# Kernel optimization log

Hardware: AMD Instinct MI355X
Metric: run time of the kernel (lower is better)

Reference implementation:

```python
import jax, jax.numpy as jnp
import numpy as np

K = 10          # n_near
BN_EPS = 1e-5   # BatchNorm eps; running stats at init: mean=0, var=1


def knn_idx(xt, k):
    # xt: [b, n, c] -> [b, n, k] indices of k nearest (incl. self)
    sq = jnp.sum(xt * xt, axis=-1)                               # [b, n]
    d = sq[:, :, None] - 2.0 * jnp.einsum('bnc,bmc->bnm', xt, xt) + sq[:, None, :]
    return jax.lax.top_k(-d, k)[1]                               # [b, n, k]


def graph_feature(x, k):
    # x: [b, c, n] -> [b, 2c, n, k]  (DGCNN edge features)
    xt = x.transpose(0, 2, 1)                                    # [b, n, c]
    idx = knn_idx(xt, k)                                         # [b, n, k]
    nei = jnp.take_along_axis(xt[:, None, :, :], idx[..., None], axis=2)  # [b, n, k, c]
    cen = xt[:, :, None, :]                                      # [b, n, 1, c]
    feat = jnp.concatenate([nei - cen, jnp.broadcast_to(cen, nei.shape)], axis=-1)
    return feat.transpose(0, 3, 1, 2)                            # [b, 2c, n, k]


def conv_bn_act(x, w, b, g, t):
    # 1x1 conv (any spatial rank) + inference BatchNorm (mean=0, var=1) + GELU
    sh = (1, -1) + (1,) * (x.ndim - 2)
    y = jnp.einsum('oi,bi...->bo...', w, x) + b.reshape(sh)
    y = y * (g.reshape(sh) / jnp.sqrt(1.0 + BN_EPS)) + t.reshape(sh)
    return jax.nn.gelu(y)


def setup_inputs() -> dict:
    key = jax.random.key(0)
    ks = jax.random.split(key, 8)
    d = {'x': jax.random.normal(ks[0], (8, 64, 2048), jnp.float32)}
    dims = {'11': (152, 128), '12': (181, 152), '21': (430, 362),
            '22': (512, 430), '31': (595, 693), '32': (512, 595)}
    for i, (tag, (o, inp)) in enumerate(dims.items()):
        d['w' + tag] = jax.random.normal(jax.random.fold_in(key, i + 1), (o, inp), jnp.float32) * 0.02
        d['b' + tag] = jnp.zeros((o,), jnp.float32)
        d['g' + tag] = jnp.ones((o,), jnp.float32)
        d['t' + tag] = jnp.zeros((o,), jnp.float32)
    return d


def reference(x, w11, b11, g11, t11, w12, b12, g12, t12,
              w21, b21, g21, t21, w22, b22, g22, t22,
              w31, b31, g31, t31, w32, b32, g32, t32):
    f = graph_feature(x, K)                       # [b, 128, n, k]
    f = conv_bn_act(f, w11, b11, g11, t11)
    f = conv_bn_act(f, w12, b12, g12, t12)        # [b, 181, n, k]
    x1 = jnp.max(f, axis=-1)                      # [b, 181, n]
    f = graph_feature(x1, K)                      # [b, 362, n, k]
    f = conv_bn_act(f, w21, b21, g21, t21)
    f = conv_bn_act(f, w22, b22, g22, t22)        # [b, 512, n, k]
    x2 = jnp.max(f, axis=-1)                      # [b, 512, n]
    f = jnp.concatenate([x1, x2], axis=1)         # [b, 693, n]
    f = conv_bn_act(f, w31, b31, g31, t31)
    f = conv_bn_act(f, w32, b32, g32, t32)        # [b, 512, n]
    return f
```

## Files before the change

kernel.cpp:

```cpp
#include <hip/hip_runtime.h>


typedef float f4 __attribute__((ext_vector_type(4)));
typedef float f32x4 __attribute__((ext_vector_type(4)));
typedef short bf16x8 __attribute__((ext_vector_type(8)));

#define BNRSQ 0.9999950000374997f

__device__ __forceinline__ float gelu_f(float x){
  float a = 0.7978845608028654f * (x + 0.044715f * x * x * x);
  float e = __expf(2.0f * a);
  float t = 1.0f - 2.0f / (e + 1.0f);
  return 0.5f * x * (1.0f + t);
}

__device__ __forceinline__ short f2b(float x){
  unsigned u = __float_as_uint(x);
  unsigned r = (u + 0x7fffu + ((u >> 16) & 1u)) >> 16;
  return (short)r;
}
__device__ __forceinline__ float b2f(short s){
  return __uint_as_float(((unsigned)(unsigned short)s) << 16);
}

__global__ void makewt_k(const float* __restrict__ W, float* __restrict__ dst,
                         int O, int Cin, int Cpad, int ld, int split){
  int id = blockIdx.x * 256 + threadIdx.x;
  if (id >= Cpad * O) return;
  int c = id / O;
  int o = id - c * O;
  float v = 0.f;
  if (c < Cin){
    float w0 = W[(size_t)o * ld + c];
    v = split ? (W[(size_t)o * ld + Cin + c] - w0) : w0;
  }
  dst[id] = v;
}

__global__ void makew12r_k(const float* __restrict__ w12, float* __restrict__ Wr){
  int id = blockIdx.x * 256 + threadIdx.x;
  if (id >= 38 * 192 * 4) return;
  int i = id & 3;
  int c = (id >> 2) % 192;
  int kq = id / 768;
  int k = kq * 4 + i;
  float v = 0.f;
  if (c < 181 && k < 152) v = w12[(size_t)c * 152 + k];
  Wr[id] = v;
}

__global__ void makewsb_k(const float* __restrict__ W, short* __restrict__ dst){
  int n = blockIdx.x;
  int k = threadIdx.x;
  if (k >= 192) return;
  short v = 0;
  if (k < 181){
    if (n < 430) v = f2b(W[(size_t)n * 362 + k]);
    else if (n >= 448 && n < 878){
      int m = n - 448;
      v = f2b(W[(size_t)m * 362 + 181 + k] - W[(size_t)m * 362 + k]);
    }
  }
  dst[(size_t)n * 192 + k] = v;
}

__global__ void makewb_k(const float* __restrict__ W, short* __restrict__ dst,
                         int N, int K, int Kpad){
  int n = blockIdx.y;
  int k = blockIdx.x * 256 + threadIdx.x;
  if (k >= Kpad) return;
  short v = 0;
  if (n < N && k < K) v = f2b(W[(size_t)n * K + k]);
  dst[(size_t)n * Kpad + k] = v;
}

__global__ __launch_bounds__(256) void transpose_k(const float* __restrict__ x, float* __restrict__ xt){
  __shared__ float tile[64][65];
  int b = blockIdx.y;
  int n0 = blockIdx.x * 64;
  int t = threadIdx.x;
  int a = t & 63, r = t >> 6;
  #pragma unroll
  for (int s = 0; s < 16; s++){
    int c = r + s * 4;
    tile[c][a] = x[((size_t)b * 64 + c) * 2048 + n0 + a];
  }
  __syncthreads();
  #pragma unroll
  for (int s = 0; s < 16; s++){
    int n = r + s * 4;
    xt[((size_t)b * 2048 + n0 + n) * 64 + a] = tile[a][n];
  }
}

__global__ __launch_bounds__(256) void sqnorm_k(const float* __restrict__ X, float* __restrict__ sq,
                                                int C, int ld, int npts){
  int gid = blockIdx.x * blockDim.x + threadIdx.x;
  int wid = gid >> 6, lane = gid & 63;
  if (wid >= npts) return;
  const float* row = X + (size_t)wid * ld;
  float s = 0.f;
  for (int c = lane; c < C; c += 64){ float v = row[c]; s += v * v; }
  #pragma unroll
  for (int off = 32; off; off >>= 1) s += __shfl_xor(s, off);
  if (lane == 0) sq[wid] = s;
}

__global__ __launch_bounds__(256) void dist_k(const float* __restrict__ X, const float* __restrict__ sq,
                                              float* __restrict__ dist, int C, int ldx){
  __shared__ float As[16][132];
  __shared__ float Bs[16][132];
  const int z = blockIdx.z;
  const float* Xb = X + (size_t)z * 2048 * ldx;
  const float* sqb = sq + (z << 11);
  float* db = dist + (size_t)z * 2048 * 2048;
  const int i0 = blockIdx.y * 128, j0 = blockIdx.x * 128;
  const int t = threadIdx.x;
  const int ti = t >> 4, tj = t & 15;
  const int r = t & 127, q8 = (t >> 7) * 8;
  float acc[2][2][4][4];
  #pragma unroll
  for (int a = 0; a < 2; a++)
    #pragma unroll
    for (int b = 0; b < 2; b++)
      #pragma unroll
      for (int u = 0; u < 4; u++)
        #pragma unroll
        for (int v = 0; v < 4; v++) acc[a][b][u][v] = 0.f;
  const float* Ag = Xb + (size_t)(i0 + r) * ldx + q8;
  const float* Bg = Xb + (size_t)(j0 + r) * ldx + q8;
  for (int c0 = 0; c0 < C; c0 += 16){
    f4 av0 = *(const f4*)(Ag + c0);
    f4 av1 = *(const f4*)(Ag + c0 + 4);
    f4 bv0 = *(const f4*)(Bg + c0);
    f4 bv1 = *(const f4*)(Bg + c0 + 4);
    __syncthreads();
    #pragma unroll
    for (int i = 0; i < 4; i++){
      As[q8 + i][r] = av0[i];  As[q8 + 4 + i][r] = av1[i];
      Bs[q8 + i][r] = bv0[i];  Bs[q8 + 4 + i][r] = bv1[i];
    }
    __syncthreads();
    #pragma unroll
    for (int k = 0; k < 16; k++){
      f4 a0 = *(const f4*)&As[k][ti * 4];
      f4 a1 = *(const f4*)&As[k][ti * 4 + 64];
      f4 b0 = *(const f4*)&Bs[k][tj * 4];
      f4 b1 = *(const f4*)&Bs[k][tj * 4 + 64];
      #pragma unroll
      for (int u = 0; u < 4; u++)
        #pragma unroll
        for (int v = 0; v < 4; v++){
          acc[0][0][u][v] += a0[u] * b0[v];
          acc[0][1][u][v] += a0[u] * b1[v];
          acc[1][0][u][v] += a1[u] * b0[v];
          acc[1][1][u][v] += a1[u] * b1[v];
        }
    }
  }
  #pragma unroll
  for (int ia = 0; ia < 2; ia++){
    #pragma unroll
    for (int u = 0; u < 4; u++){
      int i = i0 + ia * 64 + ti * 4 + u;
      float si = sqb[i];
      #pragma unroll
      for (int jb = 0; jb < 2; jb++){
        int j = j0 + jb * 64 + tj * 4;
        f4 o;
        #pragma unroll
        for (int v = 0; v < 4; v++) o[v] = si + sqb[j + v] - 2.0f * acc[ia][jb][u][v];
        *(f4*)&db[(size_t)i * 2048 + j] = o;
      }
    }
  }
}

__global__ __launch_bounds__(256) void topk_k(const float* __restrict__ dist, int* __restrict__ idxout){
  int z = blockIdx.y;
  int lane = threadIdx.x & 63;
  int row = blockIdx.x * 4 + (threadIdx.x >> 6);
  const float* d = dist + (size_t)z * 2048 * 2048 + (size_t)row * 2048;
  float v[32];
  #pragma unroll
  for (int s = 0; s < 32; s++) v[s] = d[s * 64 + lane];
  int* outp = idxout + (size_t)z * 20480 + (size_t)row * 10;
  for (int it = 0; it < 10; ++it){
    float bv = 3.0e38f; int bi = 0x7fffffff;
    #pragma unroll
    for (int s = 0; s < 32; s++){
      if (v[s] < bv){ bv = v[s]; bi = s * 64 + lane; }
    }
    #pragma unroll
    for (int off = 32; off; off >>= 1){
      float ov = __shfl_xor(bv, off);
      int   oi = __shfl_xor(bi, off);
      if (ov < bv || (ov == bv && oi < bi)){ bv = ov; bi = oi; }
    }
    #pragma unroll
    for (int s = 0; s < 32; s++) if (s * 64 + lane == bi) v[s] = 3.0e38f;
    if (lane == 0) outp[it] = bi;
  }
}

__global__ __launch_bounds__(256) void yz_k(const float* __restrict__ Amat, int C,
                                            const float* __restrict__ B1, const float* __restrict__ B2,
                                            int O, float* __restrict__ Y, float* __restrict__ Z){
  __shared__ float As[16][68];
  __shared__ float B1s[16][68];
  __shared__ float B2s[16][68];
  int m0 = blockIdx.y * 64, o0 = blockIdx.x * 64;
  int t = threadIdx.x;
  int cc = t & 15, rr = t >> 4;
  int oo = t & 63, kk = t >> 6;
  float accY[4][4], accZ[4][4];
  #pragma unroll
  for (int u = 0; u < 4; u++)
    #pragma unroll
    for (int v = 0; v < 4; v++){ accY[u][v] = 0.f; accZ[u][v] = 0.f; }
  for (int c0 = 0; c0 < C; c0 += 16){
    #pragma unroll
    for (int u = 0; u < 4; u++){
      int ii = rr + u * 16;
      As[cc][ii] = ((c0 + cc) < C) ? Amat[(size_t)(m0 + ii) * C + c0 + cc] : 0.f;
    }
    #pragma unroll
    for (int u = 0; u < 4; u++){
      int c = kk * 4 + u;
      bool ok = ((c0 + c) < C) && ((o0 + oo) < O);
      B1s[c][oo] = ok ? B1[(size_t)(c0 + c) * O + o0 + oo] : 0.f;
      B2s[c][oo] = ok ? B2[(size_t)(c0 + c) * O + o0 + oo] : 0.f;
    }
    __syncthreads();
    #pragma unroll
    for (int k = 0; k < 16; k++){
      f4 a  = *(const f4*)&As[k][rr * 4];
      f4 b1 = *(const f4*)&B1s[k][cc * 4];
      f4 b2 = *(const f4*)&B2s[k][cc * 4];
      #pragma unroll
      for (int u = 0; u < 4; u++)
        #pragma unroll
        for (int v = 0; v < 4; v++){
          accY[u][v] += a[u] * b1[v];
          accZ[u][v] += a[u] * b2[v];
        }
    }
    __syncthreads();
  }
  #pragma unroll
  for (int u = 0; u < 4; u++){
    int m = m0 + rr * 4 + u;
    #pragma unroll
    for (int v = 0; v < 4; v++){
      int o = o0 + cc * 4 + v;
      if (o < O){
        Y[(size_t)m * O + o] = accY[u][v];
        Z[(size_t)m * O + o] = accZ[u][v];
      }
    }
  }
}

__global__ __launch_bounds__(256) void fused1_k(
    const float* __restrict__ Y1, const float* __restrict__ Z1,
    const int* __restrict__ idx, const float* __restrict__ Wr12,
    const float* __restrict__ bb11, const float* __restrict__ gg11, const float* __restrict__ tt11,
    const float* __restrict__ bb12, const float* __restrict__ gg12, const float* __restrict__ tt12,
    float* __restrict__ x1t, short* __restrict__ x1b, float* __restrict__ sq2){
  __shared__ float h1[40][152];
  __shared__ int sidx[40];
  const int n0 = blockIdx.x * 4;
  const int t = threadIdx.x;
  if (t < 40) sidx[t] = idx[(size_t)n0 * 10 + t];
  __syncthreads();
  const int base = (n0 >> 11) << 11;
  {
    const int tc = t & 63, tr = t >> 6;
    for (int c = tc; c < 152; c += 64){
      float bb = bb11[c], sc = gg11[c] * BNRSQ, tb = tt11[c];
      for (int r = tr; r < 40; r += 4){
        int p = r / 10;
        int j = base + sidx[r];
        float y = Y1[(size_t)j * 152 + c] + Z1[(size_t)(n0 + p) * 152 + c];
        h1[r][c] = gelu_f((y + bb) * sc + tb);
      }
    }
  }
  __syncthreads();
  const int p = t >> 6, kh = (t >> 5) & 1, cg = t & 31;
  const int rbase = p * 10 + kh * 5;
  float acc[5][6];
  #pragma unroll
  for (int k = 0; k < 5; k++)
    #pragma unroll
    for (int j = 0; j < 6; j++) acc[k][j] = 0.f;
  for (int kq = 0; kq < 38; kq++){
    const float* wp = Wr12 + ((size_t)kq * 192 + cg) * 4;
    f4 wv[6];
    #pragma unroll
    for (int j = 0; j < 6; j++) wv[j] = *(const f4*)(wp + j * 128);
    f4 hv[5];
    #pragma unroll
    for (int k = 0; k < 5; k++) hv[k] = *(const f4*)&h1[rbase + k][kq * 4];
    #pragma unroll
    for (int k = 0; k < 5; k++)
      #pragma unroll
      for (int j = 0; j < 6; j++)
        acc[k][j] += hv[k][0] * wv[j][0] + hv[k][1] * wv[j][1]
                   + hv[k][2] * wv[j][2] + hv[k][3] * wv[j][3];
  }
  float ssum = 0.f;
  #pragma unroll
  for (int j = 0; j < 6; j++){
    int c = cg + j * 32;
    float m = 0.f;
    if (c < 181){
      float bb = bb12[c], sc = gg12[c] * BNRSQ, tb = tt12[c];
      m = -3.0e38f;
      #pragma unroll
      for (int k = 0; k < 5; k++){
        float v = gelu_f((acc[k][j] + bb) * sc + tb);
        m = fmaxf(m, v);
      }
    }
    float o = __shfl_xor(m, 32);
    m = fmaxf(m, o);
    if (kh == 0){
      float mv = (c < 181) ? m : 0.f;
      x1t[(size_t)(n0 + p) * 192 + c] = mv;
      x1b[(size_t)(n0 + p) * 192 + c] = f2b(mv);
      ssum += mv * mv;
    }
  }
  #pragma unroll
  for (int off = 16; off; off >>= 1) ssum += __shfl_xor(ssum, off);
  if (kh == 0 && cg == 0) sq2[n0 + p] = ssum;
}

__global__ __launch_bounds__(256) void h2_k(
    const float* __restrict__ YZ, const int* __restrict__ idx,
    const float* __restrict__ bb21, const float* __restrict__ gg21, const float* __restrict__ tt21,
    short* __restrict__ H2){
  __shared__ int sidx[10];
  int bl = blockIdx.x;
  int t = threadIdx.x;
  if (t < 10) sidx[t] = ((bl >> 11) << 11) + idx[(size_t)bl * 10 + t];
  __syncthreads();
  int cA = t;
  int cB = t + 256;
  float zA = YZ[(size_t)bl * 896 + 448 + cA] + bb21[cA];
  float scA = gg21[cA] * BNRSQ, tbA = tt21[cA];
  float zB = 0.f, scB = 0.f, tbB = 0.f;
  bool realB = cB < 430, padB = cB < 448;
  if (realB){
    zB = YZ[(size_t)bl * 896 + 448 + cB] + bb21[cB];
    scB = gg21[cB] * BNRSQ; tbB = tt21[cB];
  }
  #pragma unroll
  for (int k = 0; k < 10; k++){
    int nb = sidx[k];
    size_t rb = ((size_t)bl * 10 + k) * 448;
    float yA = YZ[(size_t)nb * 896 + cA] + zA;
    H2[rb + cA] = f2b(gelu_f(yA * scA + tbA));
    if (padB){
      short v = 0;
      if (realB){
        float yB = YZ[(size_t)nb * 896 + cB] + zB;
        v = f2b(gelu_f(yB * scB + tbB));
      }
      H2[rb + cB] = v;
    }
  }
}

template<int MODE>
__global__ __launch_bounds__(256) void gemm_k(const short* __restrict__ A,
                                              const short* __restrict__ Bt,
                                              int Kp, int Nld, int Nreal,
                                              const float* __restrict__ bv,
                                              const float* __restrict__ gv,
                                              const float* __restrict__ tv,
                                              void* __restrict__ outp){
  __shared__ short As[128][40];
  __shared__ short Bs[128][40];
  const int t = threadIdx.x;
  const int w = t >> 6, l = t & 63;
  const int m0 = blockIdx.y * 128, n0 = blockIdx.x * 128;
  f32x4 acc[2][8];
  #pragma unroll
  for (int i = 0; i < 2; i++)
    #pragma unroll
    for (int j = 0; j < 8; j++) acc[i][j] = (f32x4)0.f;
  const int ar = t >> 2, akc = t & 3;
  const short* Ag0 = A + (size_t)(m0 + ar) * Kp + akc * 8;
  const short* Ag1 = A + (size_t)(m0 + 64 + ar) * Kp + akc * 8;
  const short* Bg0 = Bt + (size_t)(n0 + ar) * Kp + akc * 8;
  const short* Bg1 = Bt + (size_t)(n0 + 64 + ar) * Kp + akc * 8;
  const int mrow = w * 32 + (l & 15);
  const int kg = (l >> 4) * 8;
  const int cl = l & 15;
  for (int k0 = 0; k0 < Kp; k0 += 32){
    int4 va0 = *(const int4*)(Ag0 + k0);
    int4 va1 = *(const int4*)(Ag1 + k0);
    int4 vb0 = *(const int4*)(Bg0 + k0);
    int4 vb1 = *(const int4*)(Bg1 + k0);
    __syncthreads();
    *(int4*)&As[ar][akc * 8]      = va0;
    *(int4*)&As[ar + 64][akc * 8] = va1;
    *(int4*)&Bs[ar][akc * 8]      = vb0;
    *(int4*)&Bs[ar + 64][akc * 8] = vb1;
    __syncthreads();
    bf16x8 a0 = *(const bf16x8*)&As[mrow][kg];
    bf16x8 a1 = *(const bf16x8*)&As[mrow + 16][kg];
    #pragma unroll
    for (int ni = 0; ni < 8; ni++){
      bf16x8 b = *(const bf16x8*)&Bs[cl + ni * 16][kg];
      acc[0][ni] = __builtin_amdgcn_mfma_f32_16x16x32_bf16(a0, b, acc[0][ni], 0, 0, 0);
      acc[1][ni] = __builtin_amdgcn_mfma_f32_16x16x32_bf16(a1, b, acc[1][ni], 0, 0, 0);
    }
  }
  const int rbase = (l >> 4) * 4;
  #pragma unroll
  for (int ni = 0; ni < 8; ni++){
    int n = n0 + ni * 16 + cl;
    float bb = 0.f, sc = 0.f, tb = 0.f;
    if (MODE != 2 && n < Nreal){ bb = bv[n]; sc = gv[n] * BNRSQ; tb = tv[n]; }
    #pragma unroll
    for (int mi = 0; mi < 2; mi++){
      #pragma unroll
      for (int r = 0; r < 4; r++){
        int m = m0 + w * 32 + mi * 16 + rbase + r;
        float a = acc[mi][ni][r];
        float v = (MODE == 2) ? a : gelu_f((a + bb) * sc + tb);
        if (MODE == 0) ((short*)outp)[(size_t)m * Nld + n] = f2b(v);
        else           ((float*)outp)[(size_t)m * Nld + n] = v;
      }
    }
  }
}

__global__ __launch_bounds__(256) void kmax_k(const short* __restrict__ Pb, short* __restrict__ x2b){
  int p = blockIdx.x;
  int t = threadIdx.x;
  #pragma unroll
  for (int j = 0; j < 2; j++){
    int o = t + j * 256;
    float m = -3.0e38f;
    #pragma unroll
    for (int k = 0; k < 10; k++) m = fmaxf(m, b2f(Pb[((size_t)p * 10 + k) * 512 + o]));
    x2b[(size_t)p * 512 + o] = f2b(m);
  }
}

__global__ __launch_bounds__(256) void fcat_k(const float* __restrict__ x1t, const short* __restrict__ x2b,
                                              short* __restrict__ F){
  size_t g = blockIdx.x;
  int t = threadIdx.x;
  for (int c = t; c < 704; c += 256){
    short v = 0;
    if (c < 181) v = f2b(x1t[g * 192 + c]);
    else if (c < 693) v = x2b[g * 512 + (c - 181)];
    F[g * 704 + c] = v;
  }
}

__global__ __launch_bounds__(256) void trout_k(const float* __restrict__ H6, float* __restrict__ out){
  __shared__ float tile[64][65];
  int b = blockIdx.z;
  int nc = blockIdx.x * 64, oc = blockIdx.y * 64;
  int t = threadIdx.x;
  int a = t & 63, r = t >> 6;
  #pragma unroll
  for (int s = 0; s < 16; s++){
    int nl = r + s * 4;
    tile[nl][a] = H6[((size_t)b * 2048 + nc + nl) * 512 + oc + a];
  }
  __syncthreads();
  #pragma unroll
  for (int s = 0; s < 16; s++){
    int ol = r + s * 4;
    out[((size_t)(b * 512 + oc + ol)) * 2048 + nc + a] = tile[a][ol];
  }
}

extern "C" void kernel_launch(void* const* d_in, const int* in_sizes, int n_in,
                              void* d_out, int out_size, void* d_ws, size_t ws_size,
                              hipStream_t stream) {
  const float* x   = (const float*)d_in[0];
  const float* w11 = (const float*)d_in[1];
  const float* b11 = (const float*)d_in[2];
  const float* g11 = (const float*)d_in[3];
  const float* t11 = (const float*)d_in[4];
  const float* w12 = (const float*)d_in[5];
  const float* b12 = (const float*)d_in[6];
  const float* g12 = (const float*)d_in[7];
  const float* t12 = (const float*)d_in[8];
  const float* w21 = (const float*)d_in[9];
  const float* b21 = (const float*)d_in[10];
  const float* g21 = (const float*)d_in[11];
  const float* t21 = (const float*)d_in[12];
  const float* w22 = (const float*)d_in[13];
  const float* b22 = (const float*)d_in[14];
  const float* g22 = (const float*)d_in[15];
  const float* t22 = (const float*)d_in[16];
  const float* w31 = (const float*)d_in[17];
  const float* b31 = (const float*)d_in[18];
  const float* g31 = (const float*)d_in[19];
  const float* t31 = (const float*)d_in[20];
  const float* w32 = (const float*)d_in[21];
  const float* b32 = (const float*)d_in[22];
  const float* g32 = (const float*)d_in[23];
  const float* t32 = (const float*)d_in[24];
  float* out = (float*)d_out;
  char* ws = (char*)d_ws;

  size_t off = 0;
  auto alloc = [&](size_t nbytes) -> char* {
    char* p = ws + off;
    off += ((nbytes + 255) & ~(size_t)255);
    return p;
  };
  float* x1t  = (float*)alloc((size_t)16384 * 192 * 4);
  short* x1b  = (short*)alloc((size_t)16384 * 192 * 2);
  short* x2b  = (short*)alloc((size_t)16384 * 512 * 2);
  float* sq1  = (float*)alloc(65536);
  float* sq2  = (float*)alloc(65536);
  int*   idx1 = (int*)  alloc(655360);
  int*   idx2 = (int*)  alloc(655360);
  float* WaT11 = (float*)alloc(64 * 152 * 4);
  float* WdT11 = (float*)alloc(64 * 152 * 4);
  float* Wr12  = (float*)alloc(38 * 192 * 4 * 4);
  short* W21sb = (short*)alloc((size_t)896 * 192 * 2);
  short* W22b  = (short*)alloc((size_t)512 * 448 * 2);
  short* W31b  = (short*)alloc((size_t)640 * 704 * 2);
  short* W32b  = (short*)alloc((size_t)512 * 640 * 2);
  char* arena = ws + off;
  const size_t ARENA = 93323264;
  if (off + ARENA > ws_size) return;
  float* distP = (float*)(arena);
  float* Y1    = (float*)(arena + 67108864);
  float* Z1    = (float*)(arena + 77070336);
  float* xt    = (float*)(arena + 87031808);
  short* Pb    = (short*)(arena);
  short* H2b   = (short*)(arena + 41943040);
  float* YZ2g  = (float*)(arena + 78643200);
  short* F     = (short*)(arena);
  short* H5    = (short*)(arena + 23068672);
  float* H6    = (float*)(arena + 44040192);

  auto mk = [&](const float* W, float* dst, int O, int Cin, int Cpad, int ld, int split){
    int n = Cpad * O;
    makewt_k<<<dim3((n + 255) / 256), dim3(256), 0, stream>>>(W, dst, O, Cin, Cpad, ld, split);
  };
  mk(w11, WaT11, 152, 64, 64, 128, 0);
  mk(w11, WdT11, 152, 64, 64, 128, 1);
  makew12r_k<<<dim3(114), dim3(256), 0, stream>>>(w12, Wr12);
  makewsb_k<<<dim3(896), dim3(256), 0, stream>>>(w21, W21sb);
  makewb_k<<<dim3(2, 512), dim3(256), 0, stream>>>(w22, W22b, 512, 430, 448);
  makewb_k<<<dim3(3, 640), dim3(256), 0, stream>>>(w31, W31b, 595, 693, 704);
  makewb_k<<<dim3(3, 512), dim3(256), 0, stream>>>(w32, W32b, 512, 595, 640);

  transpose_k<<<dim3(32, 8), dim3(256), 0, stream>>>(x, xt);
  sqnorm_k<<<dim3(4096), dim3(256), 0, stream>>>(xt, sq1, 64, 64, 16384);

  for (int pb = 0; pb < 2; pb++){
    dist_k<<<dim3(16, 16, 4), dim3(256), 0, stream>>>(xt + (size_t)pb * 4 * 2048 * 64,
                                                      sq1 + pb * 8192, distP, 64, 64);
    topk_k<<<dim3(512, 4), dim3(256), 0, stream>>>(distP, idx1 + (size_t)pb * 4 * 20480);
  }
  yz_k<<<dim3(3, 256), dim3(256), 0, stream>>>(xt, 64, WaT11, WdT11, 152, Y1, Z1);
  fused1_k<<<dim3(4096), dim3(256), 0, stream>>>(Y1, Z1, idx1, Wr12,
                                                 b11, g11, t11, b12, g12, t12,
                                                 x1t, x1b, sq2);

  for (int pb = 0; pb < 2; pb++){
    dist_k<<<dim3(16, 16, 4), dim3(256), 0, stream>>>(x1t + (size_t)pb * 4 * 2048 * 192,
                                                      sq2 + pb * 8192, distP, 192, 192);
    topk_k<<<dim3(512, 4), dim3(256), 0, stream>>>(distP, idx2 + (size_t)pb * 4 * 20480);
  }
  for (int g = 0; g < 4; g++){
    gemm_k<2><<<dim3(7, 32), dim3(256), 0, stream>>>(x1b + (size_t)g * 4096 * 192, W21sb,
                                                     192, 896, 896,
                                                     nullptr, nullptr, nullptr, (void*)YZ2g);
    h2_k<<<dim3(4096), dim3(256), 0, stream>>>(YZ2g, idx2 + (size_t)g * 40960,
                                               b21, g21, t21, H2b);
    gemm_k<0><<<dim3(4, 320), dim3(256), 0, stream>>>(H2b, W22b, 448, 512, 512,
                                                      b22, g22, t22, (void*)Pb);
    kmax_k<<<dim3(4096), dim3(256), 0, stream>>>(Pb, x2b + (size_t)g * 4096 * 512);
  }

  fcat_k<<<dim3(16384), dim3(256), 0, stream>>>(x1t, x2b, F);
  gemm_k<0><<<dim3(5, 128), dim3(256), 0, stream>>>(F, W31b, 704, 640, 595,
                                                    b31, g31, t31, (void*)H5);
  gemm_k<1><<<dim3(4, 128), dim3(256), 0, stream>>>(H5, W32b, 640, 512, 512,
                                                    b32, g32, t32, (void*)H6);
  trout_k<<<dim3(32, 8, 8), dim3(256), 0, stream>>>(H6, out);
}
```

Before: 1.098 ms.

## Merge weight-prep kernels into one launch, tune fused1 occupancy and use FMA chain

Seven weight-preparation launches are folded into a single prep kernel that dispatches on block index ranges, which removes per-launch overhead. fused1_k gets a launch bound asking for 4 blocks per SIMD-level occupancy, which may constrain its register allocation. Its inner dot product is rewritten as an explicit chain of fmaf calls. The FMA chain changes the order of the float summation slightly.

```diff
diff --git a/kernel.cpp b/kernel.cpp
--- a/kernel.cpp
+++ b/kernel.cpp
@@ -23,55 +23,68 @@
   return __uint_as_float(((unsigned)(unsigned short)s) << 16);
 }
 
-__global__ void makewt_k(const float* __restrict__ W, float* __restrict__ dst,
-                         int O, int Cin, int Cpad, int ld, int split){
-  int id = blockIdx.x * 256 + threadIdx.x;
-  if (id >= Cpad * O) return;
-  int c = id / O;
-  int o = id - c * O;
-  float v = 0.f;
-  if (c < Cin){
-    float w0 = W[(size_t)o * ld + c];
-    v = split ? (W[(size_t)o * ld + Cin + c] - w0) : w0;
-  }
-  dst[id] = v;
-}
-
-__global__ void makew12r_k(const float* __restrict__ w12, float* __restrict__ Wr){
-  int id = blockIdx.x * 256 + threadIdx.x;
-  if (id >= 38 * 192 * 4) return;
-  int i = id & 3;
-  int c = (id >> 2) % 192;
-  int kq = id / 768;
-  int k = kq * 4 + i;
-  float v = 0.f;
-  if (c < 181 && k < 152) v = w12[(size_t)c * 152 + k];
-  Wr[id] = v;
-}
-
-__global__ void makewsb_k(const float* __restrict__ W, short* __restrict__ dst){
-  int n = blockIdx.x;
-  int k = threadIdx.x;
-  if (k >= 192) return;
-  short v = 0;
-  if (k < 181){
-    if (n < 430) v = f2b(W[(size_t)n * 362 + k]);
-    else if (n >= 448 && n < 878){
-      int m = n - 448;
-      v = f2b(W[(size_t)m * 362 + 181 + k] - W[(size_t)m * 362 + k]);
-    }
-  }
-  dst[(size_t)n * 192 + k] = v;
-}
-
-__global__ void makewb_k(const float* __restrict__ W, short* __restrict__ dst,
-                         int N, int K, int Kpad){
-  int n = blockIdx.y;
-  int k = blockIdx.x * 256 + threadIdx.x;
-  if (k >= Kpad) return;
-  short v = 0;
-  if (n < N && k < K) v = f2b(W[(size_t)n * K + k]);
-  dst[(size_t)n * Kpad + k] = v;
+__global__ void prep_k(const float* __restrict__ w11, const float* __restrict__ w12,
+                       const float* __restrict__ w21, const float* __restrict__ w22,
+                       const float* __restrict__ w31, const float* __restrict__ w32,
+                       float* __restrict__ WaT11, float* __restrict__ WdT11,
+                       float* __restrict__ Wr12, short* __restrict__ W21sb,
+                       short* __restrict__ W22b, short* __restrict__ W31b,
+                       short* __restrict__ W32b){
+  const int bid = blockIdx.x;
+  const int t = threadIdx.x;
+  if (bid < 76){
+    int split = bid >= 38;
+    int id = (split ? bid - 38 : bid) * 256 + t;
+    if (id < 64 * 152){
+      int c = id / 152, o = id - c * 152;
+      float w0 = w11[(size_t)o * 128 + c];
+      float v = split ? (w11[(size_t)o * 128 + 64 + c] - w0) : w0;
+      (split ? WdT11 : WaT11)[id] = v;
+    }
+  } else if (bid < 190){
+    int id = (bid - 76) * 256 + t;
+    if (id < 38 * 192 * 4){
+      int i = id & 3, c = (id >> 2) % 192, kq = id / 768;
+      int k = kq * 4 + i;
+      float v = 0.f;
+      if (c < 181 && k < 152) v = w12[(size_t)c * 152 + k];
+      Wr12[id] = v;
+    }
+  } else if (bid < 1086){
+    int n = bid - 190;
+    if (t < 192){
+      short v = 0;
+      if (t < 181){
+        if (n < 430) v = f2b(w21[(size_t)n * 362 + t]);
+        else if (n >= 448 && n < 878){
+          int m = n - 448;
+          v = f2b(w21[(size_t)m * 362 + 181 + t] - w21[(size_t)m * 362 + t]);
+        }
+      }
+      W21sb[(size_t)n * 192 + t] = v;
+    }
+  } else if (bid < 1598){
+    int n = bid - 1086;
+    for (int k = t; k < 448; k += 256){
+      short v = 0;
+      if (k < 430) v = f2b(w22[(size_t)n * 430 + k]);
+      W22b[(size_t)n * 448 + k] = v;
+    }
+  } else if (bid < 2238){
+    int n = bid - 1598;
+    for (int k = t; k < 704; k += 256){
+      short v = 0;
+      if (n < 595 && k < 693) v = f2b(w31[(size_t)n * 693 + k]);
+      W31b[(size_t)n * 704 + k] = v;
+    }
+  } else {
+    int n = bid - 2238;
+    for (int k = t; k < 640; k += 256){
+      short v = 0;
+      if (k < 595) v = f2b(w32[(size_t)n * 595 + k]);
+      W32b[(size_t)n * 640 + k] = v;
+    }
+  }
 }
 
 __global__ __launch_bounds__(256) void transpose_k(const float* __restrict__ x, float* __restrict__ xt){
@@ -261,7 +274,7 @@
   }
 }
 
-__global__ __launch_bounds__(256) void fused1_k(
+__global__ __launch_bounds__(256, 4) void fused1_k(
     const float* __restrict__ Y1, const float* __restrict__ Z1,
     const int* __restrict__ idx, const float* __restrict__ Wr12,
     const float* __restrict__ bb11, const float* __restrict__ gg11, const float* __restrict__ tt11,
@@ -306,8 +319,10 @@
     for (int k = 0; k < 5; k++)
       #pragma unroll
       for (int j = 0; j < 6; j++)
-        acc[k][j] += hv[k][0] * wv[j][0] + hv[k][1] * wv[j][1]
-                   + hv[k][2] * wv[j][2] + hv[k][3] * wv[j][3];
+        acc[k][j] = fmaf(hv[k][3], wv[j][3],
+                    fmaf(hv[k][2], wv[j][2],
+                    fmaf(hv[k][1], wv[j][1],
+                    fmaf(hv[k][0], wv[j][0], acc[k][j]))));
   }
   float ssum = 0.f;
   #pragma unroll
@@ -548,17 +563,8 @@
   short* H5    = (short*)(arena + 23068672);
   float* H6    = (float*)(arena + 44040192);
 
-  auto mk = [&](const float* W, float* dst, int O, int Cin, int Cpad, int ld, int split){
-    int n = Cpad * O;
-    makewt_k<<<dim3((n + 255) / 256), dim3(256), 0, stream>>>(W, dst, O, Cin, Cpad, ld, split);
-  };
-  mk(w11, WaT11, 152, 64, 64, 128, 0);
-  mk(w11, WdT11, 152, 64, 64, 128, 1);
-  makew12r_k<<<dim3(114), dim3(256), 0, stream>>>(w12, Wr12);
-  makewsb_k<<<dim3(896), dim3(256), 0, stream>>>(w21, W21sb);
-  makewb_k<<<dim3(2, 512), dim3(256), 0, stream>>>(w22, W22b, 512, 430, 448);
-  makewb_k<<<dim3(3, 640), dim3(256), 0, stream>>>(w31, W31b, 595, 693, 704);
-  makewb_k<<<dim3(3, 512), dim3(256), 0, stream>>>(w32, W32b, 512, 595, 640);
+  prep_k<<<dim3(2750), dim3(256), 0, stream>>>(w11, w12, w21, w22, w31, w32,
+                                               WaT11, WdT11, Wr12, W21sb, W22b, W31b, W32b);
 
   transpose_k<<<dim3(32, 8), dim3(256), 0, stream>>>(x, xt);
   sqnorm_k<<<dim3(4096), dim3(256), 0, stream>>>(xt, sq1, 64, 64, 16384);
```

Result: no change. 1.109 ms (+1.0%).
